# Performance work log

Measured on AMD Instinct MI355X. Metric: run time of the kernel, lower is better.

The kernel has to match this reference:

```python
import jax, jax.numpy as jnp
import numpy as np

B, N, C, H, W = 4, 8, 256, 128, 128
D = C // 2


def setup_inputs() -> dict:
    key = jax.random.key(0)
    k1, k2, k3, k4 = jax.random.split(key, 4)
    encoded = jax.random.normal(k1, (B, C, H, W), jnp.float32)
    # bboxes = (x_center, y_center, w, h), normalized; kept strictly inside the
    # image so each ROI slice (as in the torch code) is non-empty and in-bounds.
    u = jax.random.uniform(k2, (B, N, 4), jnp.float32)
    cx = 0.3 + 0.4 * u[..., 0]
    cy = 0.3 + 0.4 * u[..., 1]
    bw = 0.1 + 0.2 * u[..., 2]
    bh = 0.1 + 0.2 * u[..., 3]
    bboxes = jnp.stack([cx, cy, bw, bh], axis=-1)
    w1 = jax.random.normal(k3, (D, C), jnp.float32) * (1.0 / np.sqrt(C))
    b1 = jnp.zeros((D,), jnp.float32)
    w2 = jax.random.normal(k4, (4, D), jnp.float32) * (1.0 / np.sqrt(D))
    b2 = jnp.zeros((4,), jnp.float32)
    return dict(encoded=encoded, bboxes=bboxes, w1=w1, b1=b1, w2=w2, b2=b2)


def reference(encoded, bboxes, w1, b1, w2, b2):
    # encoded: [B, C, H, W]; bboxes: [B, N, 4] normalized (x, y, w, h)
    Bv, Cv, Hv, Wv = encoded.shape
    xc = (bboxes[..., 0] * Wv).astype(jnp.int32)  # int(x * W)
    yc = (bboxes[..., 1] * Hv).astype(jnp.int32)
    hw = (bboxes[..., 2] * Wv).astype(jnp.int32) // 2  # w//2
    hh = (bboxes[..., 3] * Hv).astype(jnp.int32) // 2  # h//2
    cols = jnp.arange(Wv)
    rows = jnp.arange(Hv)
    # slice [c - w//2 : c + w//2 + 1] == inclusive range; rectangular ROI mask
    # is separable into a row mask and a column mask.
    mask_w = (cols >= (xc - hw)[..., None]) & (cols <= (xc + hw)[..., None])  # [B,N,W]
    mask_h = (rows >= (yc - hh)[..., None]) & (rows <= (yc + hh)[..., None])  # [B,N,H]
    neg = jnp.finfo(encoded.dtype).min
    # masked max over W, then over H (ROI max-pool)
    m1 = jnp.max(jnp.where(mask_w[:, :, None, None, :], encoded[:, None], neg), axis=-1)  # [B,N,C,H]
    pooled = jnp.max(jnp.where(mask_h[:, :, None, :], m1, neg), axis=-1)  # [B,N,C]
    h1 = pooled @ w1.T + b1          # [B,N,D]
    out = jax.nn.sigmoid(h1 @ w2.T + b2)  # [B,N,4]
    # torch code cats over boxes (dim 0) then batch (dim 1) -> [N, B, 4]
    return jnp.transpose(out, (1, 0, 2))
```

## Files before the change

### kernel.cpp

```cpp
#include <hip/hip_runtime.h>
#include <hip/hip_bf16.h>
#include <float.h>

#define B_ 4
#define N_ 8
#define C_ 256
#define H_ 128
#define W_ 128
#define D_ 128

__global__ __launch_bounds__(256) void roi_pool_kernel(
    const float* __restrict__ enc,
    const float* __restrict__ bboxes,
    float* __restrict__ pooled)
{
    const int block = blockIdx.x;
    const int box   = block >> 6;
    const int cg    = block & 63;
    const int wave  = threadIdx.x >> 6;
    const int lane  = threadIdx.x & 63;
    const int c     = cg * 4 + wave;
    const int b     = box >> 3;

    const float* bb = bboxes + box * 4;
    const int xc = (int)(bb[0] * (float)W_);
    const int yc = (int)(bb[1] * (float)H_);
    const int hw = ((int)(bb[2] * (float)W_)) / 2;
    const int hh = ((int)(bb[3] * (float)H_)) / 2;
    int x0 = xc - hw, x1 = xc + hw;
    int y0 = yc - hh, y1 = yc + hh;
    x0 = max(0, x0); x1 = min(W_ - 1, x1);
    y0 = max(0, y0); y1 = min(H_ - 1, y1);
    const int rw = x1 - x0 + 1;
    const int rh = y1 - y0 + 1;
    const int total = rw * rh;

    const float* base = enc + ((b * C_ + c) * H_ + y0) * W_ + x0;

    float m = -FLT_MAX;
    for (int idx = lane; idx < total; idx += 64) {
        const int r   = idx / rw;
        const int col = idx - r * rw;
        m = fmaxf(m, base[r * W_ + col]);
    }
    #pragma unroll
    for (int off = 32; off; off >>= 1)
        m = fmaxf(m, __shfl_down(m, off));
    if (lane == 0)
        pooled[box * C_ + c] = m;
}

__global__ __launch_bounds__(128) void mlp_kernel(
    const float* __restrict__ pooled,
    const float* __restrict__ w1,
    const float* __restrict__ b1,
    const float* __restrict__ w2,
    const float* __restrict__ b2,
    float* __restrict__ out)
{
    const int i = blockIdx.x;
    const int j = threadIdx.x;

    __shared__ float p_s[C_];
    __shared__ float h1_s[D_];

    p_s[j]        = pooled[i * C_ + j];
    p_s[j + 128]  = pooled[i * C_ + 128 + j];
    __syncthreads();

    const float4* w1v = (const float4*)(w1 + j * C_);
    const float4* pv  = (const float4*)p_s;
    float s = b1[j];
    #pragma unroll 8
    for (int k = 0; k < C_ / 4; ++k) {
        const float4 wv = w1v[k];
        const float4 pp = pv[k];
        s += wv.x * pp.x + wv.y * pp.y + wv.z * pp.z + wv.w * pp.w;
    }
    h1_s[j] = s;
    __syncthreads();

    if (threadIdx.x < 64) {
        const int lane = threadIdx.x;
        #pragma unroll
        for (int jo = 0; jo < 4; ++jo) {
            float part = h1_s[lane]      * w2[jo * D_ + lane]
                       + h1_s[lane + 64] * w2[jo * D_ + lane + 64];
            #pragma unroll
            for (int off = 32; off; off >>= 1)
                part += __shfl_down(part, off);
            if (lane == 0) {
                const int b = i >> 3;
                const int n = i & 7;
                const float v = part + b2[jo];
                out[(n * B_ + b) * 4 + jo] = 1.0f / (1.0f + expf(-v));
            }
        }
    }
}

extern "C" void kernel_launch(void* const* d_in, const int* in_sizes, int n_in,
                              void* d_out, int out_size, void* d_ws, size_t ws_size,
                              hipStream_t stream) {
    const float* encoded = (const float*)d_in[0];
    const float* bboxes  = (const float*)d_in[1];
    const float* w1      = (const float*)d_in[2];
    const float* b1      = (const float*)d_in[3];
    const float* w2      = (const float*)d_in[4];
    const float* b2      = (const float*)d_in[5];
    float* out = (float*)d_out;
    float* pooled = (float*)d_ws;

    roi_pool_kernel<<<dim3(B_ * N_ * (C_ / 4)), dim3(256), 0, stream>>>(
        encoded, bboxes, pooled);
    mlp_kernel<<<dim3(B_ * N_), dim3(128), 0, stream>>>(
        pooled, w1, b1, w2, b2, out);
}
```

Before: 110.1 us.

## Row-wise ROI scan, coalesced wave-per-row MLP, device-global pooled buffer

The ROI max loop now walks row by row with lanes striding across columns, which removes the per-element integer division. The MLP kernel changes from one thread per output row, reading a strided row of w1, to one wave per output row with coalesced float4 loads and a shuffle reduction, using 256 threads. The pooled intermediate moves from the workspace to a device-global array. For narrow ROIs, the row loop leaves many lanes idle on each row.

```diff
diff --git a/kernel.cpp b/kernel.cpp
--- a/kernel.cpp
+++ b/kernel.cpp
@@ -1,5 +1,4 @@
 #include <hip/hip_runtime.h>
-#include <hip/hip_bf16.h>
 #include <float.h>
 
 #define B_ 4
@@ -9,10 +8,11 @@
 #define W_ 128
 #define D_ 128
 
+__device__ __align__(16) float pooled_g[B_ * N_ * C_];
+
 __global__ __launch_bounds__(256) void roi_pool_kernel(
     const float* __restrict__ enc,
-    const float* __restrict__ bboxes,
-    float* __restrict__ pooled)
+    const float* __restrict__ bboxes)
 {
     const int block = blockIdx.x;
     const int box   = block >> 6;
@@ -33,55 +33,50 @@
     y0 = max(0, y0); y1 = min(H_ - 1, y1);
     const int rw = x1 - x0 + 1;
     const int rh = y1 - y0 + 1;
-    const int total = rw * rh;
 
-    const float* base = enc + ((b * C_ + c) * H_ + y0) * W_ + x0;
-
+    const float* row = enc + ((b * C_ + c) * H_ + y0) * W_ + x0;
     float m = -FLT_MAX;
-    for (int idx = lane; idx < total; idx += 64) {
-        const int r   = idx / rw;
-        const int col = idx - r * rw;
-        m = fmaxf(m, base[r * W_ + col]);
+    for (int y = 0; y < rh; ++y) {
+        for (int col = lane; col < rw; col += 64)
+            m = fmaxf(m, row[col]);
+        row += W_;
     }
     #pragma unroll
     for (int off = 32; off; off >>= 1)
         m = fmaxf(m, __shfl_down(m, off));
     if (lane == 0)
-        pooled[box * C_ + c] = m;
+        pooled_g[box * C_ + c] = m;
 }
 
-__global__ __launch_bounds__(128) void mlp_kernel(
-    const float* __restrict__ pooled,
+__global__ __launch_bounds__(256) void mlp_kernel(
     const float* __restrict__ w1,
     const float* __restrict__ b1,
     const float* __restrict__ w2,
     const float* __restrict__ b2,
     float* __restrict__ out)
 {
-    const int i = blockIdx.x;
-    const int j = threadIdx.x;
+    const int i    = blockIdx.x;
+    const int wave = threadIdx.x >> 6;
+    const int lane = threadIdx.x & 63;
 
-    __shared__ float p_s[C_];
     __shared__ float h1_s[D_];
 
-    p_s[j]        = pooled[i * C_ + j];
-    p_s[j + 128]  = pooled[i * C_ + 128 + j];
+    const float4 pp = ((const float4*)(pooled_g + i * C_))[lane];
+
+    const float4* w1v = (const float4*)w1;
+    for (int r = 0; r < 32; ++r) {
+        const int j = wave * 32 + r;
+        const float4 wv = w1v[j * 64 + lane];
+        float s = wv.x * pp.x + wv.y * pp.y + wv.z * pp.z + wv.w * pp.w;
+        #pragma unroll
+        for (int off = 32; off; off >>= 1)
+            s += __shfl_down(s, off);
+        if (lane == 0)
+            h1_s[j] = s + b1[j];
+    }
     __syncthreads();
 
-    const float4* w1v = (const float4*)(w1 + j * C_);
-    const float4* pv  = (const float4*)p_s;
-    float s = b1[j];
-    #pragma unroll 8
-    for (int k = 0; k < C_ / 4; ++k) {
-        const float4 wv = w1v[k];
-        const float4 pp = pv[k];
-        s += wv.x * pp.x + wv.y * pp.y + wv.z * pp.z + wv.w * pp.w;
-    }
-    h1_s[j] = s;
-    __syncthreads();
-
-    if (threadIdx.x < 64) {
-        const int lane = threadIdx.x;
+    if (wave == 0) {
         #pragma unroll
         for (int jo = 0; jo < 4; ++jo) {
             float part = h1_s[lane]      * w2[jo * D_ + lane]
@@ -109,10 +104,10 @@
     const float* w2      = (const float*)d_in[4];
     const float* b2      = (const float*)d_in[5];
     float* out = (float*)d_out;
-    float* pooled = (float*)d_ws;
+    (void)d_ws; (void)ws_size;
 
     roi_pool_kernel<<<dim3(B_ * N_ * (C_ / 4)), dim3(256), 0, stream>>>(
-        encoded, bboxes, pooled);
-    mlp_kernel<<<dim3(B_ * N_), dim3(128), 0, stream>>>(
-        pooled, w1, b1, w2, b2, out);
+        encoded, bboxes);
+    mlp_kernel<<<dim3(B_ * N_), dim3(256), 0, stream>>>(
+        w1, b1, w2, b2, out);
 }
```

Result: slower. 128.8 us (+16.9%).
